# Kernel tuning notes

Hardware: AMD Instinct MI355X
Metric: run time of the kernel (lower is better)

## Reference

```python
import jax, jax.numpy as jnp
import numpy as np

B, P, D = 64, 196, 768
HP = WP = 14
N_CLASSES = 200
C = N_CLASSES + 1
K_PROTO = 5
GAMMA = 0.999
TEMP = 0.2
EPS_SK = 0.05
SK_ITERS = 3


def l2norm(x, axis=-1, eps=1e-12):
    n = jnp.linalg.norm(x, axis=axis, keepdims=True)
    return x / jnp.maximum(n, eps)


def _safe_div(a, b):
    return a / jnp.where(b > 0, b, 1.0)


def masked_sinkhorn(L_cnk, mask):
    """Vectorized per-class Sinkhorn-Knopp over masked patch groups.
    L_cnk: [C, N, K] logits; mask: [C, N] bool (patch n belongs to class c).
    Returns Q: [C, K, N] (columns of each present class sum to 1)."""
    m = mask[:, None, :].astype(L_cnk.dtype)  # [C,1,N]
    Q = jnp.exp(jnp.transpose(L_cnk, (0, 2, 1)) / EPS_SK) * m  # [C,K,N]
    Q = _safe_div(Q, Q.sum(axis=(1, 2), keepdims=True))
    Nc = mask.sum(axis=1).astype(Q.dtype)[:, None, None]  # per-class patch count
    Nc_safe = jnp.where(Nc > 0, Nc, 1.0)
    for _ in range(SK_ITERS):
        Q = _safe_div(Q, Q.sum(axis=2, keepdims=True)) / K_PROTO  # row (prototype) norm
        Q = _safe_div(Q, Q.sum(axis=1, keepdims=True)) / Nc_safe  # col (patch) norm
    Q = Q * Nc  # undo final /Nc -> each patch column sums to 1
    return Q


def setup_inputs() -> dict:
    key = jax.random.key(0)
    k1, k2, k3, k4, k5 = jax.random.split(key, 5)
    patch_tokens = jax.random.normal(k1, (B, P, D), dtype=jnp.float32)
    raw_patch_tokens = jax.random.normal(k2, (B, P, D), dtype=jnp.float32)
    prototypes = 0.02 * jax.random.normal(k3, (C, K_PROTO, D), dtype=jnp.float32)
    sa_weights = jnp.full((N_CLASSES, K_PROTO), 0.5, dtype=jnp.float32)
    pseudo_patch_labels = jax.random.randint(k5, (B, HP, WP), 0, C, dtype=jnp.int32)
    return {
        "patch_tokens": patch_tokens,
        "raw_patch_tokens": raw_patch_tokens,
        "prototypes": prototypes,
        "sa_weights": sa_weights,
        "pseudo_patch_labels": pseudo_patch_labels,
    }


def reference(patch_tokens, raw_patch_tokens, prototypes, sa_weights, pseudo_patch_labels):
    # --- patch-prototype cosine similarity ---
    pt = l2norm(patch_tokens)                       # [B,P,D]
    proto_n = l2norm(prototypes)                    # [C,K,D]
    logits = jnp.einsum('bpd,ckd->bpck', pt, proto_n)  # [B,P,C,K]
    image_logits = logits.max(axis=1)               # [B,C,K]
    # --- ScoreAggregation classifier ---
    sw = jax.nn.softmax(sa_weights, axis=-1) * K_PROTO  # [n_classes,K]
    class_logits = (image_logits[:, :-1, :] * sw).sum(-1) / TEMP  # [B,n_classes]
    # --- online clustering (detached in original) ---
    rpt = l2norm(raw_patch_tokens)
    patches_flat = rpt.reshape(-1, D)               # [N,D], N=B*P
    labels_flat = pseudo_patch_labels.reshape(-1)   # [N]
    N = labels_flat.shape[0]
    L_nck = logits.reshape(N, C, K_PROTO)
    L_cnk = jnp.transpose(L_nck, (1, 0, 2))         # [C,N,K]
    mask = labels_flat[None, :] == jnp.arange(C)[:, None]  # [C,N]
    Q = masked_sinkhorn(L_cnk, mask)                # [C,K,N]
    # grouped GEMM: P_c_new = Q_c @ I_c for every class at once
    P_new_c = jnp.einsum('ckn,nd->ckd', Q, patches_flat)  # [C,K,D]
    present = mask.any(axis=1)[:, None, None]
    P_new = jnp.where(present,
                      GAMMA * prototypes + (1.0 - GAMMA) * P_new_c,
                      prototypes)
    # part assignment: argmax_k Q[label_n, k, n] + label_n * K
    Q_nck = jnp.transpose(Q, (2, 0, 1))             # [N,C,K]
    Q_at = Q_nck[jnp.arange(N), labels_flat]        # [N,K]
    assign = jnp.argmax(Q_at, axis=-1).astype(jnp.int32) + labels_flat * K_PROTO
    part_assignment_maps = assign.reshape(B, HP * WP)
    return (logits, image_logits, class_logits, part_assignment_maps, P_new)
```

## Files before the change

### kernel.cpp

```cpp
#include <hip/hip_runtime.h>
#include <math.h>

#define B_ 64
#define P_ 196
#define D_ 768
#define C_ 201
#define K_ 5
#define N_ (B_*P_)
#define CK_ (C_*K_)
#define NPAD 1024
#define NCLS 200
#define GAMMA_ 0.999f
#define INV_TEMP 5.0f
#define INV_EPS 20.0f
#define CAP2 256
#define EPAD 8
#define MTILES 98
#define ROWS_TOT (2*N_ + NPAD)

typedef short s16x8 __attribute__((ext_vector_type(8)));
typedef float f32x4 __attribute__((ext_vector_type(4)));
typedef unsigned short u16x4 __attribute__((ext_vector_type(4)));

typedef __attribute__((address_space(3))) void lds_void;
typedef __attribute__((address_space(1))) const void g_void;
#define GLD16(gp, lp) __builtin_amdgcn_global_load_lds((g_void*)(gp), (lds_void*)(lp), 16, 0, 0)

__device__ __forceinline__ unsigned short f2bf(float f) {
    unsigned int u = __float_as_uint(f);
    unsigned int r = (u + 0x7FFFu + ((u >> 16) & 1u)) >> 16;
    return (unsigned short)r;
}

__global__ __launch_bounds__(256) void norm_all_kernel(
        const float* __restrict__ patch, const float* __restrict__ rawp,
        const float* __restrict__ proto, float* __restrict__ invR,
        unsigned short* __restrict__ Abf, unsigned short* __restrict__ Bbf,
        int* __restrict__ cnt) {
    if (blockIdx.x == 0 && threadIdx.x < C_) cnt[threadIdx.x] = 0;
    int gw = blockIdx.x * 4 + (threadIdx.x >> 6);
    int lane = threadIdx.x & 63;
    const float* src; unsigned short* dst; int realR; int r; bool wantInv = false;
    if (gw < N_) { r = gw; src = patch; dst = Abf; realR = N_; }
    else if (gw < 2 * N_) { r = gw - N_; src = rawp; dst = nullptr; realR = N_; wantInv = true; }
    else { r = gw - 2 * N_; src = proto; dst = Bbf; realR = CK_; }
    unsigned short* brow = dst ? dst + (size_t)r * D_ : nullptr;
    if (r >= realR) {
        u16x4 z = (u16x4)0;
        *(u16x4*)(brow + lane * 4)       = z;
        *(u16x4*)(brow + lane * 4 + 256) = z;
        *(u16x4*)(brow + lane * 4 + 512) = z;
        return;
    }
    const float4* row4 = (const float4*)(src + (size_t)r * D_);
    float4 v0 = row4[lane], v1 = row4[lane + 64], v2 = row4[lane + 128];
    float s = v0.x*v0.x + v0.y*v0.y + v0.z*v0.z + v0.w*v0.w
            + v1.x*v1.x + v1.y*v1.y + v1.z*v1.z + v1.w*v1.w
            + v2.x*v2.x + v2.y*v2.y + v2.z*v2.z + v2.w*v2.w;
#pragma unroll
    for (int o = 1; o < 64; o <<= 1) s += __shfl_xor(s, o, 64);
    float sc = 1.f / fmaxf(sqrtf(s), 1e-12f);
    if (brow) {
        u16x4 p0 = { f2bf(v0.x*sc), f2bf(v0.y*sc), f2bf(v0.z*sc), f2bf(v0.w*sc) };
        u16x4 p1 = { f2bf(v1.x*sc), f2bf(v1.y*sc), f2bf(v1.z*sc), f2bf(v1.w*sc) };
        u16x4 p2 = { f2bf(v2.x*sc), f2bf(v2.y*sc), f2bf(v2.z*sc), f2bf(v2.w*sc) };
        *(u16x4*)(brow + lane * 4)       = p0;
        *(u16x4*)(brow + lane * 4 + 256) = p1;
        *(u16x4*)(brow + lane * 4 + 512) = p2;
    } else if (wantInv && lane == 0) invR[r] = sc;
}

#define BM 128
#define BN 128
#define BKq 32
#define KITER (D_/BKq)
#define NBUF 3
__global__ __launch_bounds__(256) void gemm_mfma_kernel(
    const unsigned short* __restrict__ Ab, const unsigned short* __restrict__ Bb,
    float* __restrict__ Cc,
    float* __restrict__ part) {
    __shared__ short As[NBUF][BM * BKq];
    __shared__ short Bs[NBUF][BN * BKq];
    __shared__ float maxw[4][2][BN];
    int tid = threadIdx.x;
    int bid = blockIdx.y * 8 + blockIdx.x;
    int swz = (bid & 7) * MTILES + (bid >> 3);
    int mtile = swz >> 3;
    int ntile = swz & 7;
    int mBase = mtile * BM;
    int nBase = ntile * BN;
    int w = tid >> 6;
    int lane = tid & 63;
    int wm = (w >> 1) * 64;
    int wn = (w & 1) * 64;
    int mrow = lane & 15;
    int kq = (lane >> 4) * 8;

    f32x4 acc[4][4];
#pragma unroll
    for (int i = 0; i < 4; ++i)
#pragma unroll
        for (int j = 0; j < 4; ++j) acc[i][j] = (f32x4)(0.f);

    int c0 = tid, c1 = tid + 256;
    const unsigned short* ga0 = Ab + (size_t)(mBase + (c0 >> 2)) * D_ + (c0 & 3) * 8;
    const unsigned short* ga1 = Ab + (size_t)(mBase + (c1 >> 2)) * D_ + (c1 & 3) * 8;
    const unsigned short* gb0 = Bb + (size_t)(nBase + (c0 >> 2)) * D_ + (c0 & 3) * 8;
    const unsigned short* gb1 = Bb + (size_t)(nBase + (c1 >> 2)) * D_ + (c1 & 3) * 8;

    auto stage = [&](int buf, int k0) {
        GLD16(ga0 + k0, &As[buf][c0 * 8]);
        GLD16(ga1 + k0, &As[buf][c1 * 8]);
        GLD16(gb0 + k0, &Bs[buf][c0 * 8]);
        GLD16(gb1 + k0, &Bs[buf][c1 * 8]);
    };

    stage(0, 0);
    stage(1, BKq);
    for (int u = 0; u < KITER; ++u) {
        if (u < KITER - 1) asm volatile("s_waitcnt vmcnt(4)" ::: "memory");
        else               asm volatile("s_waitcnt vmcnt(0)" ::: "memory");
        __builtin_amdgcn_s_barrier();
        __builtin_amdgcn_sched_barrier(0);
        if (u + 2 < KITER) stage((u + 2) % NBUF, (u + 2) * BKq);
        const short* Ac = As[u % NBUF];
        const short* Bc = Bs[u % NBUF];
        s16x8 a[4], b[4];
#pragma unroll
        for (int i = 0; i < 4; ++i)
            a[i] = *(const s16x8*)&Ac[(wm + 16 * i + mrow) * BKq + kq];
#pragma unroll
        for (int j = 0; j < 4; ++j)
            b[j] = *(const s16x8*)&Bc[(wn + 16 * j + mrow) * BKq + kq];
#pragma unroll
        for (int i = 0; i < 4; ++i)
#pragma unroll
            for (int j = 0; j < 4; ++j)
                acc[i][j] = __builtin_amdgcn_mfma_f32_16x16x32_bf16(a[i], b[j], acc[i][j], 0, 0, 0);
    }

#pragma unroll
    for (int i = 0; i < 4; ++i) {
        int gm = mBase + wm + 16 * i + (lane >> 4) * 4;
#pragma unroll
        for (int j = 0; j < 4; ++j) {
            int gn = nBase + wn + 16 * j + (lane & 15);
            if (gn < CK_) {
                Cc[(size_t)(gm + 0) * CK_ + gn] = acc[i][j][0];
                Cc[(size_t)(gm + 1) * CK_ + gn] = acc[i][j][1];
                Cc[(size_t)(gm + 2) * CK_ + gn] = acc[i][j][2];
                Cc[(size_t)(gm + 3) * CK_ + gn] = acc[i][j][3];
            }
        }
    }

    int imgA = mBase / 196;
    int rstar = 196 * (imgA + 1);
#pragma unroll
    for (int j = 0; j < 4; ++j) {
        float m0 = -INFINITY, m1 = -INFINITY;
#pragma unroll
        for (int i = 0; i < 4; ++i) {
            int gm = mBase + wm + 16 * i + (lane >> 4) * 4;
#pragma unroll
            for (int r = 0; r < 4; ++r) {
                float v = acc[i][j][r];
                if (gm + r >= rstar) m1 = fmaxf(m1, v); else m0 = fmaxf(m0, v);
            }
        }
        m0 = fmaxf(m0, __shfl_xor(m0, 16)); m0 = fmaxf(m0, __shfl_xor(m0, 32));
        m1 = fmaxf(m1, __shfl_xor(m1, 16)); m1 = fmaxf(m1, __shfl_xor(m1, 32));
        if (lane < 16) {
            maxw[w][0][wn + 16 * j + lane] = m0;
            maxw[w][1][wn + 16 * j + lane] = m1;
        }
    }
    __syncthreads();
    int s = tid >> 7, col = tid & 127, h = col >> 6;
    float vmax = fmaxf(maxw[h][s][col], maxw[h + 2][s][col]);
    part[(size_t)(mtile * 2 + s) * 1024 + nBase + col] = vmax;
}

__global__ __launch_bounds__(256) void post_kernel(
        const float* __restrict__ part, const float* __restrict__ saw,
        float* __restrict__ img, float* __restrict__ cls,
        const float* __restrict__ L, const int* __restrict__ labels,
        int* __restrict__ cnt, int* __restrict__ idxList, float* __restrict__ EList) {
    __shared__ float simg[CK_];
    if (blockIdx.x < B_) {
        int b = blockIdx.x;
        int t0 = (196 * b) >> 7;
        int t1 = (196 * b + 195) >> 7;
        for (int n = threadIdx.x; n < CK_; n += 256) {
            float m = -INFINITY;
            for (int t = t0; t <= t1; ++t) {
                int iA = (t << 7) / 196;
                int s = (iA == b) ? 0 : 1;
                m = fmaxf(m, part[(size_t)(t * 2 + s) * 1024 + n]);
            }
            img[b * CK_ + n] = m;
            simg[n] = m;
        }
        __syncthreads();
        int c = threadIdx.x;
        if (c < NCLS) {
            float w[K_];
            float mx = -INFINITY;
#pragma unroll
            for (int k = 0; k < K_; ++k) { w[k] = saw[c * K_ + k]; mx = fmaxf(mx, w[k]); }
            float ssum = 0.f;
#pragma unroll
            for (int k = 0; k < K_; ++k) { w[k] = expf(w[k] - mx); ssum += w[k]; }
            float acc = 0.f;
#pragma unroll
            for (int k = 0; k < K_; ++k)
                acc += simg[c * K_ + k] * (w[k] / ssum * (float)K_);
            cls[b * NCLS + c] = acc * INV_TEMP;
        }
    } else {
        int n = (blockIdx.x - B_) * 256 + threadIdx.x;
        if (n >= N_) return;
        int c = labels[n];
        int slot = atomicAdd(&cnt[c], 1);
        if (slot < CAP2) {
            idxList[c * CAP2 + slot] = n;
            const float* lp = L + (size_t)n * CK_ + c * K_;
            float e0 = expf(lp[0] * INV_EPS), e1 = expf(lp[1] * INV_EPS);
            float e2 = expf(lp[2] * INV_EPS), e3 = expf(lp[3] * INV_EPS);
            float e4 = expf(lp[4] * INV_EPS);
            float* ep = EList + ((size_t)c * CAP2 + slot) * EPAD;
            float4 v4 = { e0, e1, e2, e3 };
            *(float4*)ep = v4;
            ep[4] = e4;
        }
    }
}

#define NJ (CAP2/64)
__global__ __launch_bounds__(768) void sinkema_kernel(
    const int* __restrict__ cnt, const int* __restrict__ idxList,
    const float* __restrict__ EList, const float* __restrict__ invR,
    const float* __restrict__ rawP, const float* __restrict__ proto,
    float* __restrict__ outAssign, float* __restrict__ outProto) {
    int c = blockIdx.x;
    int tid = threadIdx.x;
    int Nc = cnt[c]; if (Nc > CAP2) Nc = CAP2;
    size_t protoOff = (size_t)c * K_ * D_;
    if (Nc == 0) {
        for (int i = tid; i < K_ * D_; i += 768)
            outProto[protoOff + i] = proto[protoOff + i];
        return;
    }
    __shared__ float s_w[K_][CAP2];
    __shared__ int s_idx[CAP2];
    for (int i = tid; i < CAP2; i += 768)
        s_idx[i] = (i < Nc) ? idxList[c * CAP2 + i] : 0;

    if (tid < 64) {
        int lane = tid;
        float e[NJ][K_];
        float cn[NJ];
#pragma unroll
        for (int j = 0; j < NJ; ++j) {
            int n = j * 64 + lane;
            bool v = n < Nc;
            cn[j] = v ? 1.f : 0.f;
            const float* ep = EList + ((size_t)c * CAP2 + n) * EPAD;
            float4 v4 = v ? *(const float4*)ep : make_float4(0.f, 0.f, 0.f, 0.f);
            e[j][0] = v4.x; e[j][1] = v4.y; e[j][2] = v4.z; e[j][3] = v4.w;
            e[j][4] = v ? ep[4] : 0.f;
        }
        float r[K_];
        for (int it = 0; it < 3; ++it) {
#pragma unroll
            for (int k = 0; k < K_; ++k) {
                float s = 0.f;
#pragma unroll
                for (int j = 0; j < NJ; ++j) s += e[j][k] * cn[j];
                for (int o = 32; o > 0; o >>= 1) s += __shfl_xor(s, o, 64);
                r[k] = 1.f / ((float)K_ * s);
            }
#pragma unroll
            for (int j = 0; j < NJ; ++j) {
                float t = 0.f;
#pragma unroll
                for (int k = 0; k < K_; ++k) t += e[j][k] * r[k];
                cn[j] = (j * 64 + lane < Nc) ? 1.f / ((float)Nc * t) : 0.f;
            }
        }
#pragma unroll
        for (int j = 0; j < NJ; ++j) {
            int n = j * 64 + lane;
            if (n >= Nc) continue;
            int idxn = s_idx[n];
            int kb = 0; float best = e[j][0] * r[0];
#pragma unroll
            for (int k = 1; k < K_; ++k) {
                float v = e[j][k] * r[k];
                if (v > best) { best = v; kb = k; }
            }
            outAssign[idxn] = (float)(kb + c * K_);
            float scale = cn[j] * (float)Nc * (1.0f - GAMMA_) * invR[idxn];
#pragma unroll
            for (int k = 0; k < K_; ++k)
                s_w[k][n] = e[j][k] * r[k] * scale;
        }
    }
    __syncthreads();

    float acc[K_] = {};
    int n = 0;
    for (; n + 3 < Nc; n += 4) {
        float v0 = rawP[(size_t)s_idx[n]     * D_ + tid];
        float v1 = rawP[(size_t)s_idx[n + 1] * D_ + tid];
        float v2 = rawP[(size_t)s_idx[n + 2] * D_ + tid];
        float v3 = rawP[(size_t)s_idx[n + 3] * D_ + tid];
#pragma unroll
        for (int k = 0; k < K_; ++k) {
            acc[k] = fmaf(s_w[k][n],     v0, acc[k]);
            acc[k] = fmaf(s_w[k][n + 1], v1, acc[k]);
            acc[k] = fmaf(s_w[k][n + 2], v2, acc[k]);
            acc[k] = fmaf(s_w[k][n + 3], v3, acc[k]);
        }
    }
    for (; n < Nc; ++n) {
        float v0 = rawP[(size_t)s_idx[n] * D_ + tid];
#pragma unroll
        for (int k = 0; k < K_; ++k) acc[k] = fmaf(s_w[k][n], v0, acc[k]);
    }
#pragma unroll
    for (int k = 0; k < K_; ++k) {
        size_t o = protoOff + (size_t)k * D_ + tid;
        outProto[o] = fmaf(GAMMA_, proto[o], acc[k]);
    }
}

extern "C" void kernel_launch(void* const* d_in, const int* in_sizes, int n_in,
                              void* d_out, int out_size, void* d_ws, size_t ws_size,
                              hipStream_t stream) {
    (void)in_sizes; (void)n_in; (void)out_size; (void)ws_size;
    const float* patch  = (const float*)d_in[0];
    const float* rawp   = (const float*)d_in[1];
    const float* proto  = (const float*)d_in[2];
    const float* saw    = (const float*)d_in[3];
    const int*   labels = (const int*)d_in[4];

    float* out    = (float*)d_out;
    float* logits = out;
    float* img    = out + 12606720;
    float* cls    = out + 12671040;
    float* assign = out + 12683840;
    float* pnew   = out + 12696384;

    float* ws   = (float*)d_ws;
    float* invR = ws;
    unsigned short* Abf = (unsigned short*)(ws + N_);
    unsigned short* Bbf = Abf + (size_t)N_ * D_;
    int*   cnt     = (int*)(Bbf + (size_t)NPAD * D_);
    int*   idxList = cnt + 256;
    float* EList   = (float*)(idxList + C_ * CAP2);
    float* part    = EList + (size_t)2 * C_ * K_ * CAP2;

    norm_all_kernel<<<ROWS_TOT / 4, 256, 0, stream>>>(patch, rawp, proto, invR, Abf, Bbf, cnt);
    gemm_mfma_kernel<<<dim3(NPAD / BN, MTILES), 256, 0, stream>>>(Abf, Bbf, logits, part);
    post_kernel<<<B_ + N_ / 256, 256, 0, stream>>>(part, saw, img, cls, logits, labels,
                                                   cnt, idxList, EList);
    sinkema_kernel<<<C_, 768, 0, stream>>>(cnt, idxList, EList, invR, rawp, proto,
                                           assign, pnew);
}
```

Baseline: 189.5 us.

## Fuse all stages into one persistent kernel with grid-wide barriers

Merges normalization, the MFMA GEMM, the post-processing/bucketing, and the Sinkhorn/EMA stage into a single 784-block kernel separated by atomic-counter grid barriers. A memset resets the barrier and counters. The goal is to remove three kernel launch gaps and the tail idle time between them. In exchange, the GEMM pipeline drops from triple to double buffering with full syncthreads, and the final stage runs with 256 threads instead of 768. The grid barrier also relies on all 784 blocks being co-resident, which launch_bounds(256,4) is meant to allow.

```diff
diff --git a/kernel.cpp b/kernel.cpp
--- a/kernel.cpp
+++ b/kernel.cpp
@@ -17,6 +17,7 @@
 #define EPAD 8
 #define MTILES 98
 #define ROWS_TOT (2*N_ + NPAD)
+#define NBLK 784
 
 typedef short s16x8 __attribute__((ext_vector_type(8)));
 typedef float f32x4 __attribute__((ext_vector_type(4)));
@@ -32,166 +33,175 @@
     return (unsigned short)r;
 }
 
-__global__ __launch_bounds__(256) void norm_all_kernel(
-        const float* __restrict__ patch, const float* __restrict__ rawp,
-        const float* __restrict__ proto, float* __restrict__ invR,
-        unsigned short* __restrict__ Abf, unsigned short* __restrict__ Bbf,
-        int* __restrict__ cnt) {
-    if (blockIdx.x == 0 && threadIdx.x < C_) cnt[threadIdx.x] = 0;
-    int gw = blockIdx.x * 4 + (threadIdx.x >> 6);
-    int lane = threadIdx.x & 63;
-    const float* src; unsigned short* dst; int realR; int r; bool wantInv = false;
-    if (gw < N_) { r = gw; src = patch; dst = Abf; realR = N_; }
-    else if (gw < 2 * N_) { r = gw - N_; src = rawp; dst = nullptr; realR = N_; wantInv = true; }
-    else { r = gw - 2 * N_; src = proto; dst = Bbf; realR = CK_; }
-    unsigned short* brow = dst ? dst + (size_t)r * D_ : nullptr;
-    if (r >= realR) {
-        u16x4 z = (u16x4)0;
-        *(u16x4*)(brow + lane * 4)       = z;
-        *(u16x4*)(brow + lane * 4 + 256) = z;
-        *(u16x4*)(brow + lane * 4 + 512) = z;
-        return;
-    }
-    const float4* row4 = (const float4*)(src + (size_t)r * D_);
-    float4 v0 = row4[lane], v1 = row4[lane + 64], v2 = row4[lane + 128];
-    float s = v0.x*v0.x + v0.y*v0.y + v0.z*v0.z + v0.w*v0.w
-            + v1.x*v1.x + v1.y*v1.y + v1.z*v1.z + v1.w*v1.w
-            + v2.x*v2.x + v2.y*v2.y + v2.z*v2.z + v2.w*v2.w;
-#pragma unroll
-    for (int o = 1; o < 64; o <<= 1) s += __shfl_xor(s, o, 64);
-    float sc = 1.f / fmaxf(sqrtf(s), 1e-12f);
-    if (brow) {
-        u16x4 p0 = { f2bf(v0.x*sc), f2bf(v0.y*sc), f2bf(v0.z*sc), f2bf(v0.w*sc) };
-        u16x4 p1 = { f2bf(v1.x*sc), f2bf(v1.y*sc), f2bf(v1.z*sc), f2bf(v1.w*sc) };
-        u16x4 p2 = { f2bf(v2.x*sc), f2bf(v2.y*sc), f2bf(v2.z*sc), f2bf(v2.w*sc) };
-        *(u16x4*)(brow + lane * 4)       = p0;
-        *(u16x4*)(brow + lane * 4 + 256) = p1;
-        *(u16x4*)(brow + lane * 4 + 512) = p2;
-    } else if (wantInv && lane == 0) invR[r] = sc;
+__device__ __forceinline__ void gsync(unsigned* bar, unsigned phase) {
+    __syncthreads();
+    if (threadIdx.x == 0) {
+        __threadfence();
+        unsigned old = atomicAdd(&bar[0], 1u);
+        if (old == (unsigned)NBLK * phase - 1u) {
+            atomicExch(&bar[1], phase);
+        } else {
+            while (atomicAdd(&bar[1], 0u) < phase) __builtin_amdgcn_s_sleep(2);
+        }
+        __threadfence();
+    }
+    __syncthreads();
 }
 
 #define BM 128
 #define BN 128
 #define BKq 32
-#define KITER (D_/BKq)
-#define NBUF 3
-__global__ __launch_bounds__(256) void gemm_mfma_kernel(
-    const unsigned short* __restrict__ Ab, const unsigned short* __restrict__ Bb,
-    float* __restrict__ Cc,
-    float* __restrict__ part) {
-    __shared__ short As[NBUF][BM * BKq];
-    __shared__ short Bs[NBUF][BN * BKq];
-    __shared__ float maxw[4][2][BN];
+__global__ __launch_bounds__(256, 4) void mega_kernel(
+        const float* __restrict__ patch, const float* __restrict__ rawp,
+        const float* __restrict__ proto, const float* __restrict__ saw,
+        const int* __restrict__ labels,
+        float* __restrict__ logits, float* __restrict__ img, float* __restrict__ cls,
+        float* __restrict__ assign, float* __restrict__ pnew,
+        unsigned* __restrict__ bar, int* __restrict__ cnt, float* __restrict__ invR,
+        unsigned short* __restrict__ Abf, unsigned short* __restrict__ Bbf,
+        int* __restrict__ idxList, float* __restrict__ EList, float* __restrict__ part) {
+    __shared__ union {
+        struct { short As[2][BM * BKq]; short Bs[2][BN * BKq]; float maxw[4][2][BN]; } g;
+        struct { float s_w[K_][CAP2]; int s_idx[CAP2]; } s;
+        struct { float simg[CK_]; } p;
+    } u;
+    int bid = blockIdx.x;
     int tid = threadIdx.x;
-    int bid = blockIdx.y * 8 + blockIdx.x;
-    int swz = (bid & 7) * MTILES + (bid >> 3);
-    int mtile = swz >> 3;
-    int ntile = swz & 7;
-    int mBase = mtile * BM;
-    int nBase = ntile * BN;
     int w = tid >> 6;
     int lane = tid & 63;
-    int wm = (w >> 1) * 64;
-    int wn = (w & 1) * 64;
-    int mrow = lane & 15;
-    int kq = (lane >> 4) * 8;
-
-    f32x4 acc[4][4];
-#pragma unroll
-    for (int i = 0; i < 4; ++i)
-#pragma unroll
-        for (int j = 0; j < 4; ++j) acc[i][j] = (f32x4)(0.f);
-
-    int c0 = tid, c1 = tid + 256;
-    const unsigned short* ga0 = Ab + (size_t)(mBase + (c0 >> 2)) * D_ + (c0 & 3) * 8;
-    const unsigned short* ga1 = Ab + (size_t)(mBase + (c1 >> 2)) * D_ + (c1 & 3) * 8;
-    const unsigned short* gb0 = Bb + (size_t)(nBase + (c0 >> 2)) * D_ + (c0 & 3) * 8;
-    const unsigned short* gb1 = Bb + (size_t)(nBase + (c1 >> 2)) * D_ + (c1 & 3) * 8;
-
-    auto stage = [&](int buf, int k0) {
-        GLD16(ga0 + k0, &As[buf][c0 * 8]);
-        GLD16(ga1 + k0, &As[buf][c1 * 8]);
-        GLD16(gb0 + k0, &Bs[buf][c0 * 8]);
-        GLD16(gb1 + k0, &Bs[buf][c1 * 8]);
-    };
-
-    stage(0, 0);
-    stage(1, BKq);
-    for (int u = 0; u < KITER; ++u) {
-        if (u < KITER - 1) asm volatile("s_waitcnt vmcnt(4)" ::: "memory");
-        else               asm volatile("s_waitcnt vmcnt(0)" ::: "memory");
-        __builtin_amdgcn_s_barrier();
-        __builtin_amdgcn_sched_barrier(0);
-        if (u + 2 < KITER) stage((u + 2) % NBUF, (u + 2) * BKq);
-        const short* Ac = As[u % NBUF];
-        const short* Bc = Bs[u % NBUF];
-        s16x8 a[4], b[4];
+
+    for (int gw = bid * 4 + w; gw < ROWS_TOT; gw += NBLK * 4) {
+        const float* src; unsigned short* dst; int realR; int r; bool wantInv = false;
+        if (gw < N_) { r = gw; src = patch; dst = Abf; realR = N_; }
+        else if (gw < 2 * N_) { r = gw - N_; src = rawp; dst = nullptr; realR = N_; wantInv = true; }
+        else { r = gw - 2 * N_; src = proto; dst = Bbf; realR = CK_; }
+        unsigned short* brow = dst ? dst + (size_t)r * D_ : nullptr;
+        if (r >= realR) {
+            u16x4 z = (u16x4)0;
+            *(u16x4*)(brow + lane * 4)       = z;
+            *(u16x4*)(brow + lane * 4 + 256) = z;
+            *(u16x4*)(brow + lane * 4 + 512) = z;
+            continue;
+        }
+        const float4* row4 = (const float4*)(src + (size_t)r * D_);
+        float4 v0 = row4[lane], v1 = row4[lane + 64], v2 = row4[lane + 128];
+        float s = v0.x*v0.x + v0.y*v0.y + v0.z*v0.z + v0.w*v0.w
+                + v1.x*v1.x + v1.y*v1.y + v1.z*v1.z + v1.w*v1.w
+                + v2.x*v2.x + v2.y*v2.y + v2.z*v2.z + v2.w*v2.w;
+#pragma unroll
+        for (int o = 1; o < 64; o <<= 1) s += __shfl_xor(s, o, 64);
+        float sc = 1.f / fmaxf(sqrtf(s), 1e-12f);
+        if (brow) {
+            u16x4 p0 = { f2bf(v0.x*sc), f2bf(v0.y*sc), f2bf(v0.z*sc), f2bf(v0.w*sc) };
+            u16x4 p1 = { f2bf(v1.x*sc), f2bf(v1.y*sc), f2bf(v1.z*sc), f2bf(v1.w*sc) };
+            u16x4 p2 = { f2bf(v2.x*sc), f2bf(v2.y*sc), f2bf(v2.z*sc), f2bf(v2.w*sc) };
+            *(u16x4*)(brow + lane * 4)       = p0;
+            *(u16x4*)(brow + lane * 4 + 256) = p1;
+            *(u16x4*)(brow + lane * 4 + 512) = p2;
+        } else if (wantInv && lane == 0) invR[r] = sc;
+    }
+    gsync(bar, 1);
+
+    {
+        int swz = (bid & 7) * MTILES + (bid >> 3);
+        int mtile = swz >> 3;
+        int ntile = swz & 7;
+        int mBase = mtile * BM;
+        int nBase = ntile * BN;
+        int wm = (w >> 1) * 64;
+        int wn = (w & 1) * 64;
+        int mrow = lane & 15;
+        int kq = (lane >> 4) * 8;
+
+        f32x4 acc[4][4];
 #pragma unroll
         for (int i = 0; i < 4; ++i)
-            a[i] = *(const s16x8*)&Ac[(wm + 16 * i + mrow) * BKq + kq];
-#pragma unroll
-        for (int j = 0; j < 4; ++j)
-            b[j] = *(const s16x8*)&Bc[(wn + 16 * j + mrow) * BKq + kq];
-#pragma unroll
-        for (int i = 0; i < 4; ++i)
+#pragma unroll
+            for (int j = 0; j < 4; ++j) acc[i][j] = (f32x4)(0.f);
+
+        int c0 = tid, c1 = tid + 256;
+        const unsigned short* ga0 = Abf + (size_t)(mBase + (c0 >> 2)) * D_ + (c0 & 3) * 8;
+        const unsigned short* ga1 = Abf + (size_t)(mBase + (c1 >> 2)) * D_ + (c1 & 3) * 8;
+        const unsigned short* gb0 = Bbf + (size_t)(nBase + (c0 >> 2)) * D_ + (c0 & 3) * 8;
+        const unsigned short* gb1 = Bbf + (size_t)(nBase + (c1 >> 2)) * D_ + (c1 & 3) * 8;
+
+        auto stage = [&](int buf, int k0) {
+            GLD16(ga0 + k0, &u.g.As[buf][c0 * 8]);
+            GLD16(ga1 + k0, &u.g.As[buf][c1 * 8]);
+            GLD16(gb0 + k0, &u.g.Bs[buf][c0 * 8]);
+            GLD16(gb1 + k0, &u.g.Bs[buf][c1 * 8]);
+        };
+
+        stage(0, 0);
+        __syncthreads();
+        int cur = 0;
+        for (int k0 = 0; k0 < D_; k0 += BKq) {
+            int nk = k0 + BKq;
+            if (nk < D_) stage(cur ^ 1, nk);
+            s16x8 a[4], b[4];
+#pragma unroll
+            for (int i = 0; i < 4; ++i)
+                a[i] = *(const s16x8*)&u.g.As[cur][(wm + 16 * i + mrow) * BKq + kq];
 #pragma unroll
             for (int j = 0; j < 4; ++j)
-                acc[i][j] = __builtin_amdgcn_mfma_f32_16x16x32_bf16(a[i], b[j], acc[i][j], 0, 0, 0);
-    }
-
-#pragma unroll
-    for (int i = 0; i < 4; ++i) {
-        int gm = mBase + wm + 16 * i + (lane >> 4) * 4;
-#pragma unroll
-        for (int j = 0; j < 4; ++j) {
-            int gn = nBase + wn + 16 * j + (lane & 15);
-            if (gn < CK_) {
-                Cc[(size_t)(gm + 0) * CK_ + gn] = acc[i][j][0];
-                Cc[(size_t)(gm + 1) * CK_ + gn] = acc[i][j][1];
-                Cc[(size_t)(gm + 2) * CK_ + gn] = acc[i][j][2];
-                Cc[(size_t)(gm + 3) * CK_ + gn] = acc[i][j][3];
-            }
-        }
-    }
-
-    int imgA = mBase / 196;
-    int rstar = 196 * (imgA + 1);
-#pragma unroll
-    for (int j = 0; j < 4; ++j) {
-        float m0 = -INFINITY, m1 = -INFINITY;
+                b[j] = *(const s16x8*)&u.g.Bs[cur][(wn + 16 * j + mrow) * BKq + kq];
+#pragma unroll
+            for (int i = 0; i < 4; ++i)
+#pragma unroll
+                for (int j = 0; j < 4; ++j)
+                    acc[i][j] = __builtin_amdgcn_mfma_f32_16x16x32_bf16(a[i], b[j], acc[i][j], 0, 0, 0);
+            __syncthreads();
+            cur ^= 1;
+        }
+
 #pragma unroll
         for (int i = 0; i < 4; ++i) {
             int gm = mBase + wm + 16 * i + (lane >> 4) * 4;
 #pragma unroll
-            for (int r = 0; r < 4; ++r) {
-                float v = acc[i][j][r];
-                if (gm + r >= rstar) m1 = fmaxf(m1, v); else m0 = fmaxf(m0, v);
-            }
-        }
-        m0 = fmaxf(m0, __shfl_xor(m0, 16)); m0 = fmaxf(m0, __shfl_xor(m0, 32));
-        m1 = fmaxf(m1, __shfl_xor(m1, 16)); m1 = fmaxf(m1, __shfl_xor(m1, 32));
-        if (lane < 16) {
-            maxw[w][0][wn + 16 * j + lane] = m0;
-            maxw[w][1][wn + 16 * j + lane] = m1;
-        }
-    }
-    __syncthreads();
-    int s = tid >> 7, col = tid & 127, h = col >> 6;
-    float vmax = fmaxf(maxw[h][s][col], maxw[h + 2][s][col]);
-    part[(size_t)(mtile * 2 + s) * 1024 + nBase + col] = vmax;
-}
-
-__global__ __launch_bounds__(256) void post_kernel(
-        const float* __restrict__ part, const float* __restrict__ saw,
-        float* __restrict__ img, float* __restrict__ cls,
-        const float* __restrict__ L, const int* __restrict__ labels,
-        int* __restrict__ cnt, int* __restrict__ idxList, float* __restrict__ EList) {
-    __shared__ float simg[CK_];
-    if (blockIdx.x < B_) {
-        int b = blockIdx.x;
+            for (int j = 0; j < 4; ++j) {
+                int gn = nBase + wn + 16 * j + (lane & 15);
+                if (gn < CK_) {
+                    logits[(size_t)(gm + 0) * CK_ + gn] = acc[i][j][0];
+                    logits[(size_t)(gm + 1) * CK_ + gn] = acc[i][j][1];
+                    logits[(size_t)(gm + 2) * CK_ + gn] = acc[i][j][2];
+                    logits[(size_t)(gm + 3) * CK_ + gn] = acc[i][j][3];
+                }
+            }
+        }
+
+        int imgA = mBase / 196;
+        int rstar = 196 * (imgA + 1);
+#pragma unroll
+        for (int j = 0; j < 4; ++j) {
+            float m0 = -INFINITY, m1 = -INFINITY;
+#pragma unroll
+            for (int i = 0; i < 4; ++i) {
+                int gm = mBase + wm + 16 * i + (lane >> 4) * 4;
+#pragma unroll
+                for (int r = 0; r < 4; ++r) {
+                    float v = acc[i][j][r];
+                    if (gm + r >= rstar) m1 = fmaxf(m1, v); else m0 = fmaxf(m0, v);
+                }
+            }
+            m0 = fmaxf(m0, __shfl_xor(m0, 16)); m0 = fmaxf(m0, __shfl_xor(m0, 32));
+            m1 = fmaxf(m1, __shfl_xor(m1, 16)); m1 = fmaxf(m1, __shfl_xor(m1, 32));
+            if (lane < 16) {
+                u.g.maxw[w][0][wn + 16 * j + lane] = m0;
+                u.g.maxw[w][1][wn + 16 * j + lane] = m1;
+            }
+        }
+        __syncthreads();
+        int s = tid >> 7, col = tid & 127, h = col >> 6;
+        float vmax = fmaxf(u.g.maxw[h][s][col], u.g.maxw[h + 2][s][col]);
+        part[(size_t)(mtile * 2 + s) * 1024 + nBase + col] = vmax;
+    }
+    gsync(bar, 2);
+
+    if (bid < B_) {
+        int b = bid;
         int t0 = (196 * b) >> 7;
         int t1 = (196 * b + 195) >> 7;
-        for (int n = threadIdx.x; n < CK_; n += 256) {
+        for (int n = tid; n < CK_; n += 256) {
             float m = -INFINITY;
             for (int t = t0; t <= t1; ++t) {
                 int iA = (t << 7) / 196;
@@ -199,139 +209,141 @@
                 m = fmaxf(m, part[(size_t)(t * 2 + s) * 1024 + n]);
             }
             img[b * CK_ + n] = m;
-            simg[n] = m;
+            u.p.simg[n] = m;
         }
         __syncthreads();
-        int c = threadIdx.x;
+        int c = tid;
         if (c < NCLS) {
-            float w[K_];
+            float wv[K_];
             float mx = -INFINITY;
 #pragma unroll
-            for (int k = 0; k < K_; ++k) { w[k] = saw[c * K_ + k]; mx = fmaxf(mx, w[k]); }
+            for (int k = 0; k < K_; ++k) { wv[k] = saw[c * K_ + k]; mx = fmaxf(mx, wv[k]); }
             float ssum = 0.f;
 #pragma unroll
-            for (int k = 0; k < K_; ++k) { w[k] = expf(w[k] - mx); ssum += w[k]; }
-            float acc = 0.f;
+            for (int k = 0; k < K_; ++k) { wv[k] = expf(wv[k] - mx); ssum += wv[k]; }
+            float a = 0.f;
 #pragma unroll
             for (int k = 0; k < K_; ++k)
-                acc += simg[c * K_ + k] * (w[k] / ssum * (float)K_);
-            cls[b * NCLS + c] = acc * INV_TEMP;
+                a += u.p.simg[c * K_ + k] * (wv[k] / ssum * (float)K_);
+            cls[b * NCLS + c] = a * INV_TEMP;
         }
     } else {
-        int n = (blockIdx.x - B_) * 256 + threadIdx.x;
-        if (n >= N_) return;
-        int c = labels[n];
-        int slot = atomicAdd(&cnt[c], 1);
-        if (slot < CAP2) {
-            idxList[c * CAP2 + slot] = n;
-            const float* lp = L + (size_t)n * CK_ + c * K_;
-            float e0 = expf(lp[0] * INV_EPS), e1 = expf(lp[1] * INV_EPS);
-            float e2 = expf(lp[2] * INV_EPS), e3 = expf(lp[3] * INV_EPS);
-            float e4 = expf(lp[4] * INV_EPS);
-            float* ep = EList + ((size_t)c * CAP2 + slot) * EPAD;
-            float4 v4 = { e0, e1, e2, e3 };
-            *(float4*)ep = v4;
-            ep[4] = e4;
-        }
-    }
-}
-
-#define NJ (CAP2/64)
-__global__ __launch_bounds__(768) void sinkema_kernel(
-    const int* __restrict__ cnt, const int* __restrict__ idxList,
-    const float* __restrict__ EList, const float* __restrict__ invR,
-    const float* __restrict__ rawP, const float* __restrict__ proto,
-    float* __restrict__ outAssign, float* __restrict__ outProto) {
-    int c = blockIdx.x;
-    int tid = threadIdx.x;
-    int Nc = cnt[c]; if (Nc > CAP2) Nc = CAP2;
-    size_t protoOff = (size_t)c * K_ * D_;
-    if (Nc == 0) {
-        for (int i = tid; i < K_ * D_; i += 768)
-            outProto[protoOff + i] = proto[protoOff + i];
-        return;
-    }
-    __shared__ float s_w[K_][CAP2];
-    __shared__ int s_idx[CAP2];
-    for (int i = tid; i < CAP2; i += 768)
-        s_idx[i] = (i < Nc) ? idxList[c * CAP2 + i] : 0;
-
-    if (tid < 64) {
-        int lane = tid;
-        float e[NJ][K_];
-        float cn[NJ];
-#pragma unroll
-        for (int j = 0; j < NJ; ++j) {
-            int n = j * 64 + lane;
-            bool v = n < Nc;
-            cn[j] = v ? 1.f : 0.f;
-            const float* ep = EList + ((size_t)c * CAP2 + n) * EPAD;
-            float4 v4 = v ? *(const float4*)ep : make_float4(0.f, 0.f, 0.f, 0.f);
-            e[j][0] = v4.x; e[j][1] = v4.y; e[j][2] = v4.z; e[j][3] = v4.w;
-            e[j][4] = v ? ep[4] : 0.f;
-        }
-        float r[K_];
-        for (int it = 0; it < 3; ++it) {
+        int n = (bid - B_) * 256 + tid;
+        if (n < N_) {
+            int c = labels[n];
+            int slot = atomicAdd(&cnt[c], 1);
+            if (slot < CAP2) {
+                idxList[c * CAP2 + slot] = n;
+                const float* lp = logits + (size_t)n * CK_ + c * K_;
+                float e0 = expf(lp[0] * INV_EPS), e1 = expf(lp[1] * INV_EPS);
+                float e2 = expf(lp[2] * INV_EPS), e3 = expf(lp[3] * INV_EPS);
+                float e4 = expf(lp[4] * INV_EPS);
+                float* ep = EList + ((size_t)c * CAP2 + slot) * EPAD;
+                float4 v4 = { e0, e1, e2, e3 };
+                *(float4*)ep = v4;
+                ep[4] = e4;
+            }
+        }
+    }
+    gsync(bar, 3);
+
+    if (bid < C_) {
+        int c = bid;
+        int Nc = cnt[c]; if (Nc > CAP2) Nc = CAP2;
+        size_t protoOff = (size_t)c * K_ * D_;
+        if (Nc == 0) {
+            for (int i = tid; i < K_ * D_; i += 256)
+                pnew[protoOff + i] = proto[protoOff + i];
+            return;
+        }
+        for (int i = tid; i < CAP2; i += 256)
+            u.s.s_idx[i] = (i < Nc) ? idxList[c * CAP2 + i] : 0;
+
+        if (tid < 64) {
+            int ln = tid;
+            float e[CAP2/64][K_];
+            float cn[CAP2/64];
+#pragma unroll
+            for (int j = 0; j < CAP2/64; ++j) {
+                int n = j * 64 + ln;
+                bool v = n < Nc;
+                cn[j] = v ? 1.f : 0.f;
+                const float* ep = EList + ((size_t)c * CAP2 + n) * EPAD;
+                float4 v4 = v ? *(const float4*)ep : make_float4(0.f, 0.f, 0.f, 0.f);
+                e[j][0] = v4.x; e[j][1] = v4.y; e[j][2] = v4.z; e[j][3] = v4.w;
+                e[j][4] = v ? ep[4] : 0.f;
+            }
+            float r[K_];
+            for (int it = 0; it < 3; ++it) {
+#pragma unroll
+                for (int k = 0; k < K_; ++k) {
+                    float s = 0.f;
+#pragma unroll
+                    for (int j = 0; j < CAP2/64; ++j) s += e[j][k] * cn[j];
+                    for (int o = 32; o > 0; o >>= 1) s += __shfl_xor(s, o, 64);
+                    r[k] = 1.f / ((float)K_ * s);
+                }
+#pragma unroll
+                for (int j = 0; j < CAP2/64; ++j) {
+                    float t = 0.f;
+#pragma unroll
+                    for (int k = 0; k < K_; ++k) t += e[j][k] * r[k];
+                    cn[j] = (j * 64 + ln < Nc) ? 1.f / ((float)Nc * t) : 0.f;
+                }
+            }
+#pragma unroll
+            for (int j = 0; j < CAP2/64; ++j) {
+                int n = j * 64 + ln;
+                if (n >= Nc) continue;
+                int idxn = idxList[c * CAP2 + n];
+                int kb = 0; float best = e[j][0] * r[0];
+#pragma unroll
+                for (int k = 1; k < K_; ++k) {
+                    float v = e[j][k] * r[k];
+                    if (v > best) { best = v; kb = k; }
+                }
+                assign[idxn] = (float)(kb + c * K_);
+                float scale = cn[j] * (float)Nc * (1.0f - GAMMA_) * invR[idxn];
+#pragma unroll
+                for (int k = 0; k < K_; ++k)
+                    u.s.s_w[k][n] = e[j][k] * r[k] * scale;
+            }
+        }
+        __syncthreads();
+
+        float a0[K_] = {}, a1[K_] = {}, a2[K_] = {};
+        int n = 0;
+        for (; n + 1 < Nc; n += 2) {
+            const float* rp0 = rawp + (size_t)u.s.s_idx[n] * D_;
+            const float* rp1 = rawp + (size_t)u.s.s_idx[n + 1] * D_;
+            float x0 = rp0[tid], x1 = rp0[tid + 256], x2 = rp0[tid + 512];
+            float y0 = rp1[tid], y1 = rp1[tid + 256], y2 = rp1[tid + 512];
 #pragma unroll
             for (int k = 0; k < K_; ++k) {
-                float s = 0.f;
-#pragma unroll
-                for (int j = 0; j < NJ; ++j) s += e[j][k] * cn[j];
-                for (int o = 32; o > 0; o >>= 1) s += __shfl_xor(s, o, 64);
-                r[k] = 1.f / ((float)K_ * s);
-            }
-#pragma unroll
-            for (int j = 0; j < NJ; ++j) {
-                float t = 0.f;
-#pragma unroll
-                for (int k = 0; k < K_; ++k) t += e[j][k] * r[k];
-                cn[j] = (j * 64 + lane < Nc) ? 1.f / ((float)Nc * t) : 0.f;
-            }
-        }
-#pragma unroll
-        for (int j = 0; j < NJ; ++j) {
-            int n = j * 64 + lane;
-            if (n >= Nc) continue;
-            int idxn = s_idx[n];
-            int kb = 0; float best = e[j][0] * r[0];
-#pragma unroll
-            for (int k = 1; k < K_; ++k) {
-                float v = e[j][k] * r[k];
-                if (v > best) { best = v; kb = k; }
-            }
-            outAssign[idxn] = (float)(kb + c * K_);
-            float scale = cn[j] * (float)Nc * (1.0f - GAMMA_) * invR[idxn];
-#pragma unroll
-            for (int k = 0; k < K_; ++k)
-                s_w[k][n] = e[j][k] * r[k] * scale;
-        }
-    }
-    __syncthreads();
-
-    float acc[K_] = {};
-    int n = 0;
-    for (; n + 3 < Nc; n += 4) {
-        float v0 = rawP[(size_t)s_idx[n]     * D_ + tid];
-        float v1 = rawP[(size_t)s_idx[n + 1] * D_ + tid];
-        float v2 = rawP[(size_t)s_idx[n + 2] * D_ + tid];
-        float v3 = rawP[(size_t)s_idx[n + 3] * D_ + tid];
+                float w0 = u.s.s_w[k][n], w1 = u.s.s_w[k][n + 1];
+                a0[k] = fmaf(w0, x0, a0[k]); a0[k] = fmaf(w1, y0, a0[k]);
+                a1[k] = fmaf(w0, x1, a1[k]); a1[k] = fmaf(w1, y1, a1[k]);
+                a2[k] = fmaf(w0, x2, a2[k]); a2[k] = fmaf(w1, y2, a2[k]);
+            }
+        }
+        if (n < Nc) {
+            const float* rp0 = rawp + (size_t)u.s.s_idx[n] * D_;
+            float x0 = rp0[tid], x1 = rp0[tid + 256], x2 = rp0[tid + 512];
+#pragma unroll
+            for (int k = 0; k < K_; ++k) {
+                float w0 = u.s.s_w[k][n];
+                a0[k] = fmaf(w0, x0, a0[k]);
+                a1[k] = fmaf(w0, x1, a1[k]);
+                a2[k] = fmaf(w0, x2, a2[k]);
+            }
+        }
 #pragma unroll
         for (int k = 0; k < K_; ++k) {
-            acc[k] = fmaf(s_w[k][n],     v0, acc[k]);
-            acc[k] = fmaf(s_w[k][n + 1], v1, acc[k]);
-            acc[k] = fmaf(s_w[k][n + 2], v2, acc[k]);
-            acc[k] = fmaf(s_w[k][n + 3], v3, acc[k]);
-        }
-    }
-    for (; n < Nc; ++n) {
-        float v0 = rawP[(size_t)s_idx[n] * D_ + tid];
-#pragma unroll
-        for (int k = 0; k < K_; ++k) acc[k] = fmaf(s_w[k][n], v0, acc[k]);
-    }
-#pragma unroll
-    for (int k = 0; k < K_; ++k) {
-        size_t o = protoOff + (size_t)k * D_ + tid;
-        outProto[o] = fmaf(GAMMA_, proto[o], acc[k]);
+            size_t o = protoOff + (size_t)k * D_;
+            pnew[o + tid]       = fmaf(GAMMA_, proto[o + tid],       a0[k]);
+            pnew[o + tid + 256] = fmaf(GAMMA_, proto[o + tid + 256], a1[k]);
+            pnew[o + tid + 512] = fmaf(GAMMA_, proto[o + tid + 512], a2[k]);
+        }
     }
 }
 
@@ -352,19 +364,18 @@
     float* assign = out + 12683840;
     float* pnew   = out + 12696384;
 
-    float* ws   = (float*)d_ws;
-    float* invR = ws;
-    unsigned short* Abf = (unsigned short*)(ws + N_);
+    unsigned* bar = (unsigned*)d_ws;
+    int* cnt      = (int*)((char*)d_ws + 32);
+    float* invR   = (float*)((char*)d_ws + 1056);
+    unsigned short* Abf = (unsigned short*)(invR + N_);
     unsigned short* Bbf = Abf + (size_t)N_ * D_;
-    int*   cnt     = (int*)(Bbf + (size_t)NPAD * D_);
-    int*   idxList = cnt + 256;
+    int*   idxList = (int*)(Bbf + (size_t)NPAD * D_);
     float* EList   = (float*)(idxList + C_ * CAP2);
-    float* part    = EList + (size_t)2 * C_ * K_ * CAP2;
-
-    norm_all_kernel<<<ROWS_TOT / 4, 256, 0, stream>>>(patch, rawp, proto, invR, Abf, Bbf, cnt);
-    gemm_mfma_kernel<<<dim3(NPAD / BN, MTILES), 256, 0, stream>>>(Abf, Bbf, logits, part);
-    post_kernel<<<B_ + N_ / 256, 256, 0, stream>>>(part, saw, img, cls, logits, labels,
-                                                   cnt, idxList, EList);
-    sinkema_kernel<<<C_, 768, 0, stream>>>(cnt, idxList, EList, invR, rawp, proto,
-                                           assign, pnew);
+    float* part    = EList + (size_t)C_ * CAP2 * EPAD;
+
+    hipMemsetAsync(d_ws, 0, 1056, stream);
+    mega_kernel<<<NBLK, 256, 0, stream>>>(patch, rawp, proto, saw, labels,
+                                          logits, img, cls, assign, pnew,
+                                          bar, cnt, invR, Abf, Bbf,
+                                          idxList, EList, part);
 }
```

Result: slower. 485.6 us (+156.2%).

## Enlarge GEMM tiles to 256x256x64 with swizzled LDS and XCD-aware mapping

Applied to the files above, without the earlier changes.

The logits GEMM moves from 128x128 tiles with 256 threads and triple buffering to 256x256 tiles with BK=64, 512 threads and double buffering. LDS rows are XOR-swizzled to avoid bank conflicts, work-groups are remapped per XCD, and MFMA sections get raised priority. The per-image max partials now handle up to three images per M-tile, so post_kernel indexing changes to match. A missing __syncthreads is also added in sinkema_kernel. The goal is more data reuse per LDS load and fewer work-groups, at the cost of higher register and LDS pressure and only 200 work-groups.

```diff
diff --git a/kernel.cpp b/kernel.cpp
--- a/kernel.cpp
+++ b/kernel.cpp
@@ -15,7 +15,6 @@
 #define INV_EPS 20.0f
 #define CAP2 256
 #define EPAD 8
-#define MTILES 98
 #define ROWS_TOT (2*N_ + NPAD)
 
 typedef short s16x8 __attribute__((ext_vector_type(8)));
@@ -70,115 +69,155 @@
     } else if (wantInv && lane == 0) invR[r] = sc;
 }
 
-#define BM 128
-#define BN 128
-#define BKq 32
-#define KITER (D_/BKq)
-#define NBUF 3
-__global__ __launch_bounds__(256) void gemm_mfma_kernel(
+#define BM2 256
+#define BN2 256
+#define BK2 64
+#define KT (D_/BK2)
+#define MT2 (N_/BM2)
+__global__ __launch_bounds__(512, 2) void gemm_mfma_kernel(
     const unsigned short* __restrict__ Ab, const unsigned short* __restrict__ Bb,
     float* __restrict__ Cc,
     float* __restrict__ part) {
-    __shared__ short As[NBUF][BM * BKq];
-    __shared__ short Bs[NBUF][BN * BKq];
-    __shared__ float maxw[4][2][BN];
+    __shared__ union {
+        struct { short A[2][BM2 * BK2]; short B[2][BN2 * BK2]; } g;
+        float mw[2][3][BN2];
+    } u;
     int tid = threadIdx.x;
-    int bid = blockIdx.y * 8 + blockIdx.x;
-    int swz = (bid & 7) * MTILES + (bid >> 3);
-    int mtile = swz >> 3;
-    int ntile = swz & 7;
-    int mBase = mtile * BM;
-    int nBase = ntile * BN;
-    int w = tid >> 6;
+    int wid = tid >> 6;
     int lane = tid & 63;
-    int wm = (w >> 1) * 64;
-    int wn = (w & 1) * 64;
-    int mrow = lane & 15;
-    int kq = (lane >> 4) * 8;
-
-    f32x4 acc[4][4];
-#pragma unroll
-    for (int i = 0; i < 4; ++i)
+    int wr = wid >> 2, wc = wid & 3;
+    int mrow = lane & 15, q = lane >> 4;
+    int slot0 = q ^ (mrow & 7);
+
+    int orig = blockIdx.x;
+    int xcd = orig & 7, idx = orig >> 3;
+    int wg = (xcd < 4 ? xcd * 25 : 100 + (xcd - 4) * 24) + idx;
+    int mtile = wg >> 2, ntile = wg & 3;
+    int mBase = mtile * BM2;
+    int nBase = ntile * BN2;
+
+    f32x4 acc[8][4];
+#pragma unroll
+    for (int i = 0; i < 8; ++i)
 #pragma unroll
         for (int j = 0; j < 4; ++j) acc[i][j] = (f32x4)(0.f);
 
-    int c0 = tid, c1 = tid + 256;
-    const unsigned short* ga0 = Ab + (size_t)(mBase + (c0 >> 2)) * D_ + (c0 & 3) * 8;
-    const unsigned short* ga1 = Ab + (size_t)(mBase + (c1 >> 2)) * D_ + (c1 & 3) * 8;
-    const unsigned short* gb0 = Bb + (size_t)(nBase + (c0 >> 2)) * D_ + (c0 & 3) * 8;
-    const unsigned short* gb1 = Bb + (size_t)(nBase + (c1 >> 2)) * D_ + (c1 & 3) * 8;
-
-    auto stage = [&](int buf, int k0) {
-        GLD16(ga0 + k0, &As[buf][c0 * 8]);
-        GLD16(ga1 + k0, &As[buf][c1 * 8]);
-        GLD16(gb0 + k0, &Bs[buf][c0 * 8]);
-        GLD16(gb1 + k0, &Bs[buf][c1 * 8]);
+    const unsigned short* gA[4];
+    const unsigned short* gB[4];
+    int lof[4];
+#pragma unroll
+    for (int s = 0; s < 4; ++s) {
+        int c = tid + 512 * s;
+        int row = c >> 3, ch = c & 7;
+        int chx = ch ^ (row & 7);
+        gA[s] = Ab + (size_t)(mBase + row) * D_ + chx * 8;
+        gB[s] = Bb + (size_t)(nBase + row) * D_ + chx * 8;
+        lof[s] = c * 8;
+    }
+    auto stage = [&](int buf, int t) {
+#pragma unroll
+        for (int s = 0; s < 4; ++s) GLD16(gA[s] + t * BK2, &u.g.A[buf][lof[s]]);
+#pragma unroll
+        for (int s = 0; s < 4; ++s) GLD16(gB[s] + t * BK2, &u.g.B[buf][lof[s]]);
     };
 
     stage(0, 0);
-    stage(1, BKq);
-    for (int u = 0; u < KITER; ++u) {
-        if (u < KITER - 1) asm volatile("s_waitcnt vmcnt(4)" ::: "memory");
-        else               asm volatile("s_waitcnt vmcnt(0)" ::: "memory");
+    stage(1, 1);
+
+    for (int t = 0; t < KT; ++t) {
+        int cb = t & 1;
+        if (t + 1 < KT) asm volatile("s_waitcnt vmcnt(8)" ::: "memory");
+        else            asm volatile("s_waitcnt vmcnt(0)" ::: "memory");
         __builtin_amdgcn_s_barrier();
         __builtin_amdgcn_sched_barrier(0);
-        if (u + 2 < KITER) stage((u + 2) % NBUF, (u + 2) * BKq);
-        const short* Ac = As[u % NBUF];
-        const short* Bc = Bs[u % NBUF];
-        s16x8 a[4], b[4];
-#pragma unroll
-        for (int i = 0; i < 4; ++i)
-            a[i] = *(const s16x8*)&Ac[(wm + 16 * i + mrow) * BKq + kq];
-#pragma unroll
-        for (int j = 0; j < 4; ++j)
-            b[j] = *(const s16x8*)&Bc[(wn + 16 * j + mrow) * BKq + kq];
-#pragma unroll
-        for (int i = 0; i < 4; ++i)
-#pragma unroll
-            for (int j = 0; j < 4; ++j)
-                acc[i][j] = __builtin_amdgcn_mfma_f32_16x16x32_bf16(a[i], b[j], acc[i][j], 0, 0, 0);
-    }
-
-#pragma unroll
-    for (int i = 0; i < 4; ++i) {
-        int gm = mBase + wm + 16 * i + (lane >> 4) * 4;
+        const short* Ac = u.g.A[cb];
+        const short* Bc = u.g.B[cb];
+#pragma unroll
+        for (int mh = 0; mh < 2; ++mh)
+#pragma unroll
+        for (int nh = 0; nh < 2; ++nh) {
+            s16x8 a[4][2], b[2][2];
+#pragma unroll
+            for (int mf = 0; mf < 4; ++mf) {
+                int row = wr * 128 + (mh * 4 + mf) * 16 + mrow;
+                a[mf][0] = *(const s16x8*)&Ac[row * 64 + slot0 * 8];
+                a[mf][1] = *(const s16x8*)&Ac[row * 64 + (slot0 ^ 4) * 8];
+            }
+#pragma unroll
+            for (int nf = 0; nf < 2; ++nf) {
+                int row = wc * 64 + (nh * 2 + nf) * 16 + mrow;
+                b[nf][0] = *(const s16x8*)&Bc[row * 64 + slot0 * 8];
+                b[nf][1] = *(const s16x8*)&Bc[row * 64 + (slot0 ^ 4) * 8];
+            }
+            __builtin_amdgcn_s_setprio(1);
+#pragma unroll
+            for (int mf = 0; mf < 4; ++mf)
+#pragma unroll
+            for (int nf = 0; nf < 2; ++nf) {
+                acc[mh*4+mf][nh*2+nf] = __builtin_amdgcn_mfma_f32_16x16x32_bf16(
+                    a[mf][0], b[nf][0], acc[mh*4+mf][nh*2+nf], 0, 0, 0);
+                acc[mh*4+mf][nh*2+nf] = __builtin_amdgcn_mfma_f32_16x16x32_bf16(
+                    a[mf][1], b[nf][1], acc[mh*4+mf][nh*2+nf], 0, 0, 0);
+            }
+            __builtin_amdgcn_s_setprio(0);
+        }
+        asm volatile("s_waitcnt lgkmcnt(0)" ::: "memory");
+        __builtin_amdgcn_s_barrier();
+        __builtin_amdgcn_sched_barrier(0);
+        if (t + 2 < KT) stage(cb, t + 2);
+    }
+
+#pragma unroll
+    for (int m = 0; m < 8; ++m) {
+        int gm = mBase + wr * 128 + m * 16 + q * 4;
 #pragma unroll
         for (int j = 0; j < 4; ++j) {
-            int gn = nBase + wn + 16 * j + (lane & 15);
+            int gn = nBase + wc * 64 + j * 16 + mrow;
             if (gn < CK_) {
-                Cc[(size_t)(gm + 0) * CK_ + gn] = acc[i][j][0];
-                Cc[(size_t)(gm + 1) * CK_ + gn] = acc[i][j][1];
-                Cc[(size_t)(gm + 2) * CK_ + gn] = acc[i][j][2];
-                Cc[(size_t)(gm + 3) * CK_ + gn] = acc[i][j][3];
+                Cc[(size_t)(gm + 0) * CK_ + gn] = acc[m][j][0];
+                Cc[(size_t)(gm + 1) * CK_ + gn] = acc[m][j][1];
+                Cc[(size_t)(gm + 2) * CK_ + gn] = acc[m][j][2];
+                Cc[(size_t)(gm + 3) * CK_ + gn] = acc[m][j][3];
             }
         }
     }
 
     int imgA = mBase / 196;
-    int rstar = 196 * (imgA + 1);
+    int rs1 = 196 * (imgA + 1) - mBase;
+    int rs2 = rs1 + 196;
 #pragma unroll
     for (int j = 0; j < 4; ++j) {
-        float m0 = -INFINITY, m1 = -INFINITY;
-#pragma unroll
-        for (int i = 0; i < 4; ++i) {
-            int gm = mBase + wm + 16 * i + (lane >> 4) * 4;
+        float m0 = -INFINITY, m1 = -INFINITY, m2 = -INFINITY;
+#pragma unroll
+        for (int m = 0; m < 8; ++m) {
+            int lr = wr * 128 + m * 16 + q * 4;
 #pragma unroll
             for (int r = 0; r < 4; ++r) {
-                float v = acc[i][j][r];
-                if (gm + r >= rstar) m1 = fmaxf(m1, v); else m0 = fmaxf(m0, v);
+                float v = acc[m][j][r];
+                int row = lr + r;
+                if (row >= rs2) m2 = fmaxf(m2, v);
+                else if (row >= rs1) m1 = fmaxf(m1, v);
+                else m0 = fmaxf(m0, v);
             }
         }
         m0 = fmaxf(m0, __shfl_xor(m0, 16)); m0 = fmaxf(m0, __shfl_xor(m0, 32));
         m1 = fmaxf(m1, __shfl_xor(m1, 16)); m1 = fmaxf(m1, __shfl_xor(m1, 32));
+        m2 = fmaxf(m2, __shfl_xor(m2, 16)); m2 = fmaxf(m2, __shfl_xor(m2, 32));
         if (lane < 16) {
-            maxw[w][0][wn + 16 * j + lane] = m0;
-            maxw[w][1][wn + 16 * j + lane] = m1;
+            int col = wc * 64 + j * 16 + lane;
+            u.mw[wr][0][col] = m0;
+            u.mw[wr][1][col] = m1;
+            u.mw[wr][2][col] = m2;
         }
     }
     __syncthreads();
-    int s = tid >> 7, col = tid & 127, h = col >> 6;
-    float vmax = fmaxf(maxw[h][s][col], maxw[h + 2][s][col]);
-    part[(size_t)(mtile * 2 + s) * 1024 + nBase + col] = vmax;
+    if (tid < BN2) {
+#pragma unroll
+        for (int s = 0; s < 3; ++s) {
+            float vmax = fmaxf(u.mw[0][s][tid], u.mw[1][s][tid]);
+            part[(size_t)(mtile * 3 + s) * 1024 + nBase + tid] = vmax;
+        }
+    }
 }
 
 __global__ __launch_bounds__(256) void post_kernel(
@@ -189,14 +228,14 @@
     __shared__ float simg[CK_];
     if (blockIdx.x < B_) {
         int b = blockIdx.x;
-        int t0 = (196 * b) >> 7;
-        int t1 = (196 * b + 195) >> 7;
+        int t0 = (196 * b) >> 8;
+        int t1 = (196 * b + 195) >> 8;
         for (int n = threadIdx.x; n < CK_; n += 256) {
             float m = -INFINITY;
             for (int t = t0; t <= t1; ++t) {
-                int iA = (t << 7) / 196;
-                int s = (iA == b) ? 0 : 1;
-                m = fmaxf(m, part[(size_t)(t * 2 + s) * 1024 + n]);
+                int iA = (t << 8) / 196;
+                int s = b - iA;
+                m = fmaxf(m, part[(size_t)(t * 3 + s) * 1024 + n]);
             }
             img[b * CK_ + n] = m;
             simg[n] = m;
@@ -255,6 +294,7 @@
     __shared__ int s_idx[CAP2];
     for (int i = tid; i < CAP2; i += 768)
         s_idx[i] = (i < Nc) ? idxList[c * CAP2 + i] : 0;
+    __syncthreads();
 
     if (tid < 64) {
         int lane = tid;
@@ -362,7 +402,7 @@
     float* part    = EList + (size_t)2 * C_ * K_ * CAP2;
 
     norm_all_kernel<<<ROWS_TOT / 4, 256, 0, stream>>>(patch, rawp, proto, invR, Abf, Bbf, cnt);
-    gemm_mfma_kernel<<<dim3(NPAD / BN, MTILES), 256, 0, stream>>>(Abf, Bbf, logits, part);
+    gemm_mfma_kernel<<<MT2 * 4, 512, 0, stream>>>(Abf, Bbf, logits, part);
     post_kernel<<<B_ + N_ / 256, 256, 0, stream>>>(part, saw, img, cls, logits, labels,
                                                    cnt, idxList, EList);
     sinkema_kernel<<<C_, 768, 0, stream>>>(cnt, idxList, EList, invR, rawp, proto,
```

After: 183.0 us. 3.5% less time.
